# Kernel optimization log

Hardware: AMD Instinct MI355X
Metric: run time of the kernel (lower is better)

## Reference

```python
import jax, jax.numpy as jnp
import numpy as np
from jax import lax

H, W = 1024, 2048
WIN = (3, 3)            # eps=1.5 on the integer grid == 8-neighborhood (3x3 window)
MIN_SAMPLES = 4         # sklearn DBSCAN counts the point itself
MIN_CLUSTER = 30        # clusters smaller than this become noise
N_SLOTS = 26            # output channels
INT32_MAX = np.iinfo(np.int32).max


def setup_inputs() -> dict:
    key = jax.random.key(0)
    mask = jax.random.normal(key, (H, W), dtype=jnp.float32)
    return {"mask": mask}


def _minpool(x):
    # 3x3 min over int32 labels, SAME padding with +inf identity
    return lax.reduce_window(x, INT32_MAX, lax.min, WIN, (1, 1), 'SAME')


def _forward(mask):
    h, w = mask.shape
    hw = h * w
    BIG = jnp.int32(hw)  # sentinel label for 'not in any cluster'

    active = mask > 0.1
    # neighbor count in 3x3 (includes self) -> DBSCAN core condition
    cnt = lax.reduce_window(active.astype(jnp.int32), 0, lax.add, WIN, (1, 1), 'SAME')
    core = active & (cnt >= MIN_SAMPLES)

    idx2d = jnp.arange(hw, dtype=jnp.int32).reshape(h, w)
    L0 = jnp.where(core, idx2d, BIG)

    # connected components over core pixels: min-label hook (3x3 min-pool)
    # + pointer jumping (path compression) until fixpoint
    def body(st):
        L, _ = st
        Ln = jnp.where(core, jnp.minimum(L, _minpool(L)), BIG)
        flat = Ln.ravel()
        table = jnp.concatenate([flat, jnp.array([hw], jnp.int32)])  # BIG -> BIG
        flat = table[table[flat]]  # two pointer-jump hops
        Ln = flat.reshape(h, w)
        return Ln, jnp.all(Ln == L)

    def cond(st):
        return jnp.logical_not(st[1])

    L, _ = lax.while_loop(cond, body, (L0, jnp.array(False)))

    # border points: active non-core pixels with a core neighbor join the
    # (deterministically min-labeled) neighboring core cluster
    pooled = _minpool(L)
    final = jnp.where(core, L, jnp.where(active & (pooled < BIG), pooled, BIG))

    flatL = final.ravel()
    labeled = flatL < BIG
    ids = jnp.where(labeled, flatL, hw)  # noise -> extra bucket hw

    sizes = jax.ops.segment_sum(labeled.astype(jnp.int32), ids, num_segments=hw + 1)[:hw]
    col = jnp.broadcast_to(jnp.arange(w, dtype=jnp.float32), (h, w)).ravel()
    colsum = jax.ops.segment_sum(jnp.where(labeled, col, 0.0), ids, num_segments=hw + 1)[:hw]

    valid = sizes >= MIN_CLUSTER  # size filter (loc.sum() < 30 -> noise)
    means = jnp.where(valid, colsum / jnp.maximum(sizes, 1), jnp.inf)
    order = jnp.argsort(means)  # valid clusters first, sorted by mean column
    rank = jnp.zeros(hw, jnp.int32).at[order].set(jnp.arange(hw, dtype=jnp.int32))

    lab = jnp.where(labeled, flatL, 0)
    ch = rank[lab]
    pix_ok = labeled & valid[lab] & (ch < N_SLOTS)
    ch2d = jnp.where(pix_ok, ch, N_SLOTS).reshape(h, w)  # N_SLOTS == 'no channel'
    # scatter 1s into the rank-th channel
    return (ch2d[None] == jnp.arange(N_SLOTS, dtype=jnp.int32)[:, None, None]).astype(jnp.uint8)


def reference(mask):
    return _forward(mask)
```

## Files before the change

kernel.cpp:

```cpp
#include <hip/hip_runtime.h>
#include <stdint.h>

#define HH 1024
#define WW 2048
#define HWN (HH*WW)
#define BIGL HWN
#define NSLOTS 26
#define MINCL 30
#define THREADS 256
#define MAXCAND 70000
#define HSZ 512
#define TILE 4096
#define NTILES 512

__device__ __forceinline__ int uf_load(int* p, int i) {
    return __hip_atomic_load(&p[i], __ATOMIC_RELAXED, __HIP_MEMORY_SCOPE_AGENT);
}
__device__ __forceinline__ void uf_store(int* p, int i, int v) {
    __hip_atomic_store(&p[i], v, __ATOMIC_RELAXED, __HIP_MEMORY_SCOPE_AGENT);
}
__device__ int uf_find(int* parent, int x) {
    int p = uf_load(parent, x);
    while (p != x) {
        int gp = uf_load(parent, p);
        if (gp != p) uf_store(parent, x, gp);
        x = p; p = gp;
    }
    return p;
}
__device__ void uf_union(int* parent, int a, int b) {
    int ra = uf_find(parent, a);
    int rb = uf_find(parent, b);
    while (ra != rb) {
        if (ra > rb) { int t = ra; ra = rb; rb = t; }
        int old = atomicCAS(&parent[rb], rb, ra);
        if (old == rb) return;
        rb = uf_find(parent, old);
        ra = uf_find(parent, ra);
    }
}

__device__ __forceinline__ int l_load(int* p, int i) {
    return __hip_atomic_load(&p[i], __ATOMIC_RELAXED, __HIP_MEMORY_SCOPE_WORKGROUP);
}
__device__ __forceinline__ void l_store(int* p, int i, int v) {
    __hip_atomic_store(&p[i], v, __ATOMIC_RELAXED, __HIP_MEMORY_SCOPE_WORKGROUP);
}
__device__ int l_find(int* lp, int x) {
    int p = l_load(lp, x);
    while (p != x) {
        int gp = l_load(lp, p);
        if (gp != p) l_store(lp, x, gp);
        x = p; p = gp;
    }
    return p;
}
__device__ void l_union(int* lp, int a, int b) {
    int ra = l_find(lp, a);
    int rb = l_find(lp, b);
    while (ra != rb) {
        if (ra > rb) { int t = ra; ra = rb; rb = t; }
        int old = atomicCAS(&lp[rb], rb, ra);
        if (old == rb) return;
        rb = l_find(lp, old);
        ra = l_find(lp, ra);
    }
}

__global__ __launch_bounds__(THREADS) void k_init(const float* __restrict__ mask,
                                                  uint8_t* __restrict__ flags) {
    int i = blockIdx.x * THREADS + threadIdx.x;
    int r = i >> 11, c = i & (WW - 1);
    bool act = mask[i] > 0.1f;
    int cnt = 0;
    #pragma unroll
    for (int dr = -1; dr <= 1; ++dr) {
        int rr = r + dr;
        if (rr < 0 || rr >= HH) continue;
        #pragma unroll
        for (int dc = -1; dc <= 1; ++dc) {
            int cc = c + dc;
            if (cc < 0 || cc >= WW) continue;
            cnt += (mask[rr * WW + cc] > 0.1f) ? 1 : 0;
        }
    }
    bool core = act && (cnt >= 4);
    flags[i] = (uint8_t)((act ? 1 : 0) | (core ? 2 : 0));
}

__global__ __launch_bounds__(THREADS) void k_local(const uint8_t* __restrict__ flags,
                                                   int* __restrict__ parent) {
    __shared__ uint8_t lc8[TILE];
    __shared__ int lp[TILE];
    int tile_x = blockIdx.x & 31, tile_y = blockIdx.x >> 5;
    int r0 = tile_y << 6, c0 = tile_x << 6;
    {
        int row = threadIdx.x >> 2, chunk = threadIdx.x & 3;
        const uint4* src = (const uint4*)(flags + (size_t)(r0 + row) * WW + c0);
        ((uint4*)lc8)[row * 4 + chunk] = src[chunk];
    }
    for (int li = threadIdx.x; li < TILE; li += THREADS) lp[li] = li;
    __syncthreads();
    for (int li = threadIdx.x; li < TILE; li += THREADS) {
        if (!(lc8[li] & 2)) continue;
        int lr = li >> 6, lc = li & 63;
        if (lc > 0 && (lc8[li - 1] & 2)) l_union(lp, li, li - 1);
        if (lr > 0) {
            if (lc > 0  && (lc8[li - 65] & 2)) l_union(lp, li, li - 65);
            if (           (lc8[li - 64] & 2)) l_union(lp, li, li - 64);
            if (lc < 63 && (lc8[li - 63] & 2)) l_union(lp, li, li - 63);
        }
    }
    __syncthreads();
    for (int li = threadIdx.x; li < TILE; li += THREADS) {
        if (!(lc8[li] & 2)) continue;
        int root = li, p;
        while ((p = lp[root]) != root) root = p;
        int gi = (r0 + (li >> 6)) * WW + c0 + (li & 63);
        int gr = (r0 + (root >> 6)) * WW + c0 + (root & 63);
        parent[gi] = gr;
    }
}

__global__ __launch_bounds__(THREADS) void k_merge(const uint8_t* __restrict__ flags,
                                                   int* __restrict__ parent) {
    int tile_x = blockIdx.x & 31, tile_y = blockIdx.x >> 5;
    int r0 = tile_y << 6, c0 = tile_x << 6;
    int t = threadIdx.x;
    int lr, lc;
    if (t < 64)       { lr = 0;       lc = t;  }
    else if (t < 127) { lr = t - 63;  lc = 0;  }
    else if (t < 190) { lr = t - 126; lc = 63; }
    else return;
    int r = r0 + lr, c = c0 + lc;
    int i = r * WW + c;
    if (!(flags[i] & 2)) return;
    if (lc == 0 && c > 0 && (flags[i - 1] & 2))
        uf_union(parent, i, i - 1);
    if (r > 0) {
        if (lr == 0 && (flags[i - WW] & 2))
            uf_union(parent, i, i - WW);
        if ((lr == 0 || lc == 0) && c > 0 && (flags[i - WW - 1] & 2))
            uf_union(parent, i, i - WW - 1);
        if ((lr == 0 || lc == 63) && c < WW - 1 && (flags[i - WW + 1] & 2))
            uf_union(parent, i, i - WW + 1);
    }
}

__global__ __launch_bounds__(THREADS) void k_flatten(const uint8_t* __restrict__ flags,
                                                     int* __restrict__ parent,
                                                     int* __restrict__ finalL) {
    int i = blockIdx.x * THREADS + threadIdx.x;
    finalL[i] = (flags[i] & 2) ? uf_find(parent, i) : BIGL;
}

__global__ __launch_bounds__(THREADS) void k_border_stats(
        const uint8_t* __restrict__ flags, const int* __restrict__ finalL,
        int* __restrict__ labfull, int* __restrict__ sizes,
        unsigned long long* __restrict__ colsum) {
    __shared__ int h_lab[HSZ];
    __shared__ int h_sz[HSZ];
    __shared__ unsigned long long h_cs[HSZ];
    for (int t = threadIdx.x; t < HSZ; t += THREADS) {
        h_lab[t] = -1; h_sz[t] = 0; h_cs[t] = 0;
    }
    __syncthreads();

    int i = blockIdx.x * THREADS + threadIdx.x;
    int f = flags[i];
    int lab = BIGL;
    if (f & 2) {
        lab = finalL[i];
    } else if (f & 1) {
        int r = i >> 11, c = i & (WW - 1);
        int m = BIGL;
        #pragma unroll
        for (int dr = -1; dr <= 1; ++dr) {
            int rr = r + dr;
            if (rr < 0 || rr >= HH) continue;
            #pragma unroll
            for (int dc = -1; dc <= 1; ++dc) {
                int cc = c + dc;
                if (cc < 0 || cc >= WW) continue;
                int v = finalL[rr * WW + cc];
                if (v < m) m = v;
            }
        }
        lab = m;
    }
    labfull[i] = lab;

    int lane = threadIdx.x & 63;
    int labp = __shfl_up(lab, 1);
    bool head = (lane == 0) || (labp != lab);
    unsigned long long hm = __ballot(head);
    if (head && lab < BIGL) {
        unsigned long long rest = (hm >> lane) >> 1;
        int len = rest ? __ffsll((unsigned long long)rest) : (64 - lane);
        long long c0 = (long long)(i & (WW - 1));
        unsigned long long csum =
            (unsigned long long)(c0 * len + (long long)len * (len - 1) / 2);
        unsigned slot = (((unsigned)lab * 2654435761u) >> 20) & (HSZ - 1);
        for (;;) {
            int old = atomicCAS(&h_lab[slot], -1, lab);
            if (old == -1 || old == lab) {
                atomicAdd(&h_sz[slot], len);
                atomicAdd(&h_cs[slot], csum);
                break;
            }
            slot = (slot + 1) & (HSZ - 1);
        }
    }
    __syncthreads();
    for (int t = threadIdx.x; t < HSZ; t += THREADS) {
        int lb = h_lab[t];
        if (lb >= 0) {
            atomicAdd(&sizes[lb], h_sz[t]);
            atomicAdd(&colsum[lb], h_cs[t]);
        }
    }
}

__global__ __launch_bounds__(THREADS) void k_cands(const int* __restrict__ sizes,
                                                   const unsigned long long* __restrict__ colsum,
                                                   unsigned long long* __restrict__ cand,
                                                   int* __restrict__ counter) {
    int i = blockIdx.x * THREADS + threadIdx.x;
    int s = sizes[i];
    if (s >= MINCL) {
        float mean = (float)colsum[i] / (float)s;
        unsigned int mb = __float_as_uint(mean);
        unsigned long long key = ((unsigned long long)mb << 32) | (unsigned int)i;
        int p = atomicAdd(counter, 1);
        cand[p] = key;
    }
}

__global__ __launch_bounds__(1024) void k_select(const unsigned long long* __restrict__ cand,
                                                 const int* __restrict__ counter,
                                                 signed char* __restrict__ chan) {
    __shared__ unsigned long long sm[1024];
    const int tid = threadIdx.x;
    const int n = *counter;
    unsigned long long prev = 0;
    for (int k = 0; k < NSLOTS; ++k) {
        unsigned long long local = ~0ull;
        for (int j = tid; j < n; j += 1024) {
            unsigned long long v = cand[j];
            if ((k == 0 || v > prev) && v < local) local = v;
        }
        sm[tid] = local;
        __syncthreads();
        for (int s = 512; s > 0; s >>= 1) {
            if (tid < s && sm[tid + s] < sm[tid]) sm[tid] = sm[tid + s];
            __syncthreads();
        }
        unsigned long long best = sm[0];
        __syncthreads();
        if (best == ~0ull) break;
        if (tid == 0) chan[(unsigned int)(best & 0xFFFFFFFFull)] = (signed char)k;
        prev = best;
    }
}

__global__ __launch_bounds__(THREADS) void k_output(const int* __restrict__ labfull,
                                                    const signed char* __restrict__ chan,
                                                    int* __restrict__ out) {
    int i4 = (blockIdx.x * THREADS + threadIdx.x) * 4;
    int chv[4];
    #pragma unroll
    for (int t = 0; t < 4; ++t) {
        int lab = labfull[i4 + t];
        chv[t] = (lab < BIGL) ? (int)chan[lab] : -1;
    }
    #pragma unroll
    for (int c = 0; c < NSLOTS; ++c) {
        int4 v;
        v.x = (chv[0] == c) ? 1 : 0;
        v.y = (chv[1] == c) ? 1 : 0;
        v.z = (chv[2] == c) ? 1 : 0;
        v.w = (chv[3] == c) ? 1 : 0;
        *(int4*)(out + (size_t)c * HWN + i4) = v;
    }
}

extern "C" void kernel_launch(void* const* d_in, const int* in_sizes, int n_in,
                              void* d_out, int out_size, void* d_ws, size_t ws_size,
                              hipStream_t stream) {
    const float* mask = (const float*)d_in[0];
    int* out = (int*)d_out;

    char* w = (char*)d_ws;
    int* parent                 = (int*)(w);
    int* finalL                 = (int*)(w + (size_t)HWN * 4);
    int* sizes                  = (int*)(w + (size_t)HWN * 8);
    unsigned long long* colsum  = (unsigned long long*)(w + (size_t)HWN * 12);
    uint8_t* flags              = (uint8_t*)(w + (size_t)HWN * 20);
    signed char* chan           = (signed char*)(w + (size_t)HWN * 21);
    unsigned long long* cand    = (unsigned long long*)(w + (size_t)HWN * 22);
    int* counter                = (int*)(w + (size_t)HWN * 22 + MAXCAND * 8);

    hipMemsetAsync(sizes, 0, (size_t)HWN * 4, stream);
    hipMemsetAsync(colsum, 0, (size_t)HWN * 8, stream);
    hipMemsetAsync(chan, 0xFF, (size_t)HWN, stream);
    hipMemsetAsync(counter, 0, 4, stream);

    const int blocks = HWN / THREADS;
    k_init        <<<blocks, THREADS, 0, stream>>>(mask, flags);
    k_local       <<<NTILES, THREADS, 0, stream>>>(flags, parent);
    k_merge       <<<NTILES, THREADS, 0, stream>>>(flags, parent);
    k_flatten     <<<blocks, THREADS, 0, stream>>>(flags, parent, finalL);
    k_border_stats<<<blocks, THREADS, 0, stream>>>(flags, finalL, parent, sizes, colsum);
    k_cands       <<<blocks, THREADS, 0, stream>>>(sizes, colsum, cand, counter);
    k_select      <<<1, 1024, 0, stream>>>(cand, counter, chan);
    k_output      <<<HWN / (4 * THREADS), THREADS, 0, stream>>>(parent, chan, out);
}
```

Measured before the change: 436.5 us.

## Fuse core-flag computation into tile CCL and drop flatten pass

Core-flag computation (3x3 active count) moves into the tile-local union-find kernel using a shared-memory halo tile, which removes the separate init kernel and its global flag reload. The flatten kernel is removed: border_stats now calls find on parent directly for core pixels and for core neighbours of border pixels, and writes labels into a separate labfull buffer instead of reusing parent. The tile-boundary merge now skips redundant unions, using warp shuffles to dedupe runs of identical root pairs and skipping diagonal unions implied by straight neighbours. This cuts kernel launches and global traffic, at the cost of repeated find calls in border_stats.

```diff
diff --git a/kernel.cpp b/kernel.cpp
--- a/kernel.cpp
+++ b/kernel.cpp
@@ -67,40 +67,42 @@
     }
 }
 
-__global__ __launch_bounds__(THREADS) void k_init(const float* __restrict__ mask,
-                                                  uint8_t* __restrict__ flags) {
-    int i = blockIdx.x * THREADS + threadIdx.x;
-    int r = i >> 11, c = i & (WW - 1);
-    bool act = mask[i] > 0.1f;
-    int cnt = 0;
-    #pragma unroll
-    for (int dr = -1; dr <= 1; ++dr) {
-        int rr = r + dr;
-        if (rr < 0 || rr >= HH) continue;
-        #pragma unroll
-        for (int dc = -1; dc <= 1; ++dc) {
-            int cc = c + dc;
-            if (cc < 0 || cc >= WW) continue;
-            cnt += (mask[rr * WW + cc] > 0.1f) ? 1 : 0;
-        }
-    }
-    bool core = act && (cnt >= 4);
-    flags[i] = (uint8_t)((act ? 1 : 0) | (core ? 2 : 0));
-}
-
-__global__ __launch_bounds__(THREADS) void k_local(const uint8_t* __restrict__ flags,
+__global__ __launch_bounds__(THREADS) void k_local(const float* __restrict__ mask,
+                                                   uint8_t* __restrict__ flags,
                                                    int* __restrict__ parent) {
+    __shared__ uint8_t lact[66 * 72];
     __shared__ uint8_t lc8[TILE];
     __shared__ int lp[TILE];
     int tile_x = blockIdx.x & 31, tile_y = blockIdx.x >> 5;
     int r0 = tile_y << 6, c0 = tile_x << 6;
+    int tx = threadIdx.x & 15, ty = threadIdx.x >> 4;
+    for (int yy = ty; yy < 66; yy += 16) {
+        int gr = r0 - 1 + yy;
+        for (int xx = tx; xx < 66; xx += 16) {
+            int gc = c0 - 1 + xx;
+            bool a = false;
+            if ((unsigned)gr < HH && (unsigned)gc < WW)
+                a = mask[gr * WW + gc] > 0.1f;
+            lact[yy * 72 + xx] = a ? 1 : 0;
+        }
+    }
+    __syncthreads();
+    for (int li = threadIdx.x; li < TILE; li += THREADS) {
+        int lr = li >> 6, lc = li & 63;
+        int b = (lr + 1) * 72 + (lc + 1);
+        int a = lact[b];
+        int cnt = lact[b - 73] + lact[b - 72] + lact[b - 71]
+                + lact[b - 1]  + a           + lact[b + 1]
+                + lact[b + 71] + lact[b + 72] + lact[b + 73];
+        lc8[li] = (uint8_t)(a | ((a && cnt >= 4) ? 2 : 0));
+        lp[li] = li;
+    }
+    __syncthreads();
     {
         int row = threadIdx.x >> 2, chunk = threadIdx.x & 3;
-        const uint4* src = (const uint4*)(flags + (size_t)(r0 + row) * WW + c0);
-        ((uint4*)lc8)[row * 4 + chunk] = src[chunk];
-    }
-    for (int li = threadIdx.x; li < TILE; li += THREADS) lp[li] = li;
-    __syncthreads();
+        ((uint4*)(flags + (size_t)(r0 + row) * WW + c0))[chunk] =
+            ((const uint4*)lc8)[row * 4 + chunk];
+    }
     for (int li = threadIdx.x; li < TILE; li += THREADS) {
         if (!(lc8[li] & 2)) continue;
         int lr = li >> 6, lc = li & 63;
@@ -127,35 +129,68 @@
     int tile_x = blockIdx.x & 31, tile_y = blockIdx.x >> 5;
     int r0 = tile_y << 6, c0 = tile_x << 6;
     int t = threadIdx.x;
-    int lr, lc;
-    if (t < 64)       { lr = 0;       lc = t;  }
-    else if (t < 127) { lr = t - 63;  lc = 0;  }
-    else if (t < 190) { lr = t - 126; lc = 63; }
-    else return;
-    int r = r0 + lr, c = c0 + lc;
-    int i = r * WW + c;
-    if (!(flags[i] & 2)) return;
-    if (lc == 0 && c > 0 && (flags[i - 1] & 2))
-        uf_union(parent, i, i - 1);
-    if (r > 0) {
-        if (lr == 0 && (flags[i - WW] & 2))
-            uf_union(parent, i, i - WW);
-        if ((lr == 0 || lc == 0) && c > 0 && (flags[i - WW - 1] & 2))
-            uf_union(parent, i, i - WW - 1);
-        if ((lr == 0 || lc == 63) && c < WW - 1 && (flags[i - WW + 1] & 2))
-            uf_union(parent, i, i - WW + 1);
-    }
-}
-
-__global__ __launch_bounds__(THREADS) void k_flatten(const uint8_t* __restrict__ flags,
-                                                     int* __restrict__ parent,
-                                                     int* __restrict__ finalL) {
-    int i = blockIdx.x * THREADS + threadIdx.x;
-    finalL[i] = (flags[i] & 2) ? uf_find(parent, i) : BIGL;
+    int lane = t & 63;
+
+    if (t < 64) {
+        int r = r0, c = c0 + t, i = r * WW + c;
+        bool selfC = (flags[i] & 2) != 0;
+        bool nC = false, nwC = false, neC = false;
+        if (selfC && r > 0) {
+            nC  = (flags[i - WW] & 2) != 0;
+            nwC = (c > 0)      && (flags[i - WW - 1] & 2);
+            neC = (c < WW - 1) && (flags[i - WW + 1] & 2);
+        }
+        int did = 0, ra = -1, rb = -1;
+        if (selfC && r > 0 && nC) { ra = uf_find(parent, i); rb = uf_find(parent, i - WW); did = 1; }
+        int pra = __shfl_up(ra, 1), prb = __shfl_up(rb, 1), pdid = __shfl_up(did, 1);
+        bool head = (lane == 0) || !pdid || pra != ra || prb != rb;
+        if (did && head) uf_union(parent, ra, rb);
+        if (selfC && r > 0) {
+            if (t == 0) {
+                if (nwC) uf_union(parent, i, i - WW - 1);
+                if (!nC && neC) uf_union(parent, i, i - WW + 1);
+            } else if (t == 63) {
+                if (!nC && nwC) uf_union(parent, i, i - WW - 1);
+                if (neC) {
+                    bool eC = (c < WW - 1) && (flags[i + 1] & 2);
+                    if (!eC) uf_union(parent, i, i - WW + 1);
+                }
+            } else if (!nC) {
+                if (nwC) uf_union(parent, i, i - WW - 1);
+                if (neC) uf_union(parent, i, i - WW + 1);
+            }
+        }
+        if (t == 0 && selfC && c > 0 && (flags[i - 1] & 2))
+            uf_union(parent, i, i - 1);
+    } else if (t < 127) {
+        int lr = t - 63;
+        int r = r0 + lr, c = c0, i = r * WW + c;
+        bool selfC = (flags[i] & 2) != 0;
+        bool wC = false, nwC = false;
+        if (selfC && c > 0) {
+            wC  = (flags[i - 1] & 2) != 0;
+            nwC = (flags[i - WW - 1] & 2) != 0;
+        }
+        int did = 0, ra = -1, rb = -1;
+        if (selfC && wC) { ra = uf_find(parent, i); rb = uf_find(parent, i - 1); did = 1; }
+        int pra = __shfl_up(ra, 1), prb = __shfl_up(rb, 1), pdid = __shfl_up(did, 1);
+        bool head = (lane == 0) || !pdid || pra != ra || prb != rb;
+        if (did && head) uf_union(parent, ra, rb);
+        if (selfC && !wC && nwC) uf_union(parent, i, i - WW - 1);
+    } else if (t < 190) {
+        int lr = t - 126;
+        int r = r0 + lr, c = c0 + 63, i = r * WW + c;
+        bool selfC = (flags[i] & 2) != 0;
+        if (selfC && c < WW - 1) {
+            bool neC = (flags[i - WW + 1] & 2) != 0;
+            bool eC  = (flags[i + 1] & 2) != 0;
+            if (neC && !eC) uf_union(parent, i, i - WW + 1);
+        }
+    }
 }
 
 __global__ __launch_bounds__(THREADS) void k_border_stats(
-        const uint8_t* __restrict__ flags, const int* __restrict__ finalL,
+        const uint8_t* __restrict__ flags, int* __restrict__ parent,
         int* __restrict__ labfull, int* __restrict__ sizes,
         unsigned long long* __restrict__ colsum) {
     __shared__ int h_lab[HSZ];
@@ -170,7 +205,7 @@
     int f = flags[i];
     int lab = BIGL;
     if (f & 2) {
-        lab = finalL[i];
+        lab = uf_find(parent, i);
     } else if (f & 1) {
         int r = i >> 11, c = i & (WW - 1);
         int m = BIGL;
@@ -182,8 +217,11 @@
             for (int dc = -1; dc <= 1; ++dc) {
                 int cc = c + dc;
                 if (cc < 0 || cc >= WW) continue;
-                int v = finalL[rr * WW + cc];
-                if (v < m) m = v;
+                int n = rr * WW + cc;
+                if (flags[n] & 2) {
+                    int v = uf_find(parent, n);
+                    if (v < m) m = v;
+                }
             }
         }
         lab = m;
@@ -292,7 +330,7 @@
 
     char* w = (char*)d_ws;
     int* parent                 = (int*)(w);
-    int* finalL                 = (int*)(w + (size_t)HWN * 4);
+    int* labfull                = (int*)(w + (size_t)HWN * 4);
     int* sizes                  = (int*)(w + (size_t)HWN * 8);
     unsigned long long* colsum  = (unsigned long long*)(w + (size_t)HWN * 12);
     uint8_t* flags              = (uint8_t*)(w + (size_t)HWN * 20);
@@ -306,12 +344,10 @@
     hipMemsetAsync(counter, 0, 4, stream);
 
     const int blocks = HWN / THREADS;
-    k_init        <<<blocks, THREADS, 0, stream>>>(mask, flags);
-    k_local       <<<NTILES, THREADS, 0, stream>>>(flags, parent);
+    k_local       <<<NTILES, THREADS, 0, stream>>>(mask, flags, parent);
     k_merge       <<<NTILES, THREADS, 0, stream>>>(flags, parent);
-    k_flatten     <<<blocks, THREADS, 0, stream>>>(flags, parent, finalL);
-    k_border_stats<<<blocks, THREADS, 0, stream>>>(flags, finalL, parent, sizes, colsum);
+    k_border_stats<<<blocks, THREADS, 0, stream>>>(flags, parent, labfull, sizes, colsum);
     k_cands       <<<blocks, THREADS, 0, stream>>>(sizes, colsum, cand, counter);
     k_select      <<<1, 1024, 0, stream>>>(cand, counter, chan);
-    k_output      <<<HWN / (4 * THREADS), THREADS, 0, stream>>>(parent, chan, out);
-}
+    k_output      <<<HWN / (4 * THREADS), THREADS, 0, stream>>>(labfull, chan, out);
+}
```

New measurement: 423.3 us. 1.03x faster.
